# Kernel optimization log

Measured on AMD Instinct MI355X. Metric: run time of the kernel, lower is better.

The kernel has to match this reference:

```python
import jax, jax.numpy as jnp
import numpy as np

NEG_INF = -9e15  # matches torch reference mask value
LEAKY_SLOPE = 0.2  # alpha passed to nn.LeakyReLU


def setup_inputs() -> dict:
    key = jax.random.key(0)
    k1, k2, k3 = jax.random.split(key, 3)
    B, N, E = 256, 300, 100
    item_embeddings = jax.random.normal(k1, (B, N, E), dtype=jnp.float32)
    adj = jax.random.randint(k2, (B, N, N), 0, 5, dtype=jnp.int64)  # edge types 0..4
    A = jax.random.normal(k3, (4, E), dtype=jnp.float32)  # stacked a_0..a_3
    return {"item_embeddings": item_embeddings, "adj": adj, "A": A}


def reference(item_embeddings, adj, A):
    h = item_embeddings  # [B, N, E]
    # Original: a_input[b,i,j,:] = h[b,i,:] * h[b,j,:]; e_k = leakyrelu(a_input @ a_k).
    # Equivalent without the (B,N,N,E) tensor: e_k[b,i,j] = lrelu(sum_d h[b,i,d] h[b,j,d] A[k,d]).
    e = jnp.einsum('bid,bjd,kd->kbij', h, h, A)  # [4, B, N, N]
    e = jax.nn.leaky_relu(e, LEAKY_SLOPE)
    mask = jnp.full_like(e[0], NEG_INF)
    alpha = jnp.where(adj == 1, e[0], mask)
    alpha = jnp.where(adj == 2, e[1], alpha)
    alpha = jnp.where(adj == 3, e[2], alpha)
    alpha = jnp.where(adj == 4, e[3], alpha)
    alpha = jax.nn.softmax(alpha, axis=-1)
    return jnp.matmul(alpha, h)  # [B, N, E]
```

## Files before the change

kernel.cpp:

```cpp
#include <hip/hip_runtime.h>


typedef _Float16 half8 __attribute__((ext_vector_type(8)));
typedef _Float16 half4 __attribute__((ext_vector_type(4)));
typedef float f32x4 __attribute__((ext_vector_type(4)));

constexpr int B_ = 256, N_ = 300, E_ = 100;
constexpr float NEGINF = -9e15f;
constexpr float PADV   = -3e38f;

constexpr int LDS_BYTES = 68096 + 1024;

__global__ __launch_bounds__(640)
void gat_flash6(const float* __restrict__ H, const int* __restrict__ ADJ,
                const float* __restrict__ A, float* __restrict__ OUT) {
  extern __shared__ char smraw[];
  _Float16* hS  = (_Float16*)smraw;
  _Float16* A16 = (_Float16*)(smraw + 68096);

  const int bid = blockIdx.x;
  const int b = bid >> 1, q = bid & 1;
  const int tid = threadIdx.x;
  const int w = tid >> 6, lane = tid & 63;
  const int lg = lane >> 4, ll = lane & 15;

  const float* Hb  = H + (size_t)b * (N_ * E_);
  const int*   AJb = ADJ + (size_t)b * (N_ * N_);

  for (int u = tid; u < 304 * 14; u += 640) {
    const int j = u / 14, hr = u % 14;
    half8 v;
#pragma unroll
    for (int e = 0; e < 8; ++e) {
      const int d = hr * 8 + e;
      v[e] = (_Float16)((j < N_ && d < E_) ? Hb[j * E_ + d] : 0.f);
    }
    *(half8*)&hS[(((j >> 4) * 7 + (hr >> 1)) << 8) + ((j & 15) << 4) + ((hr & 1) << 3)] = v;
  }
  if (tid < 64) {
    const int k = tid >> 4, oct = tid & 15;
    half8 v;
#pragma unroll
    for (int e = 0; e < 8; ++e) {
      const int d = oct * 8 + e;
      v[e] = (_Float16)((d < E_) ? A[k * E_ + d] : 0.f);
    }
    *(half8*)&A16[k * 128 + oct * 8] = v;
  }
  __syncthreads();

  const unsigned ldsbase = (unsigned)(size_t)(void*)hS;
  const unsigned trlane  = (unsigned)(ll * 8 + lg * 128);

  const int s = 2 * w + q;
  if (s < 19) {
    const int irow = s * 16 + ll;
    const int irc  = irow < N_ ? irow : N_ - 1;

    half8 g[3][4];
    half4 gt[4];
#pragma unroll
    for (int db = 0; db < 3; ++db) {
      const int doct = db * 4 + lg;
      const half8 hi = *(const half8*)&hS[((s * 7 + (doct >> 1)) << 8) + (ll << 4) + ((doct & 1) << 3)];
#pragma unroll
      for (int k = 0; k < 4; ++k)
        g[db][k] = hi * *(const half8*)&A16[k * 128 + doct * 8];
    }
    {
      const half4 hit = *(const half4*)&hS[((s * 7 + 6) << 8) + (ll << 4) + lg * 4];
#pragma unroll
      for (int k = 0; k < 4; ++k)
        gt[k] = hit * *(const half4*)&A16[k * 128 + 96 + lg * 4];
    }

    float m = PADV, lsum = 0.f;
    f32x4 acc[7];
#pragma unroll
    for (int t = 0; t < 7; ++t) acc[t] = (f32x4){0.f, 0.f, 0.f, 0.f};

    const int* ajrow = AJb + (size_t)irc * N_;
    int4 av = *(const int4*)(ajrow + lg * 4);

    for (int jt = 0; jt < 19; ++jt) {
      int4 avn = av;
      if (jt < 18) {
        int jc = jt * 16 + 16 + lg * 4;
        if (jc > N_ - 4) jc = N_ - 4;
        avn = *(const int4*)(ajrow + jc);
      }

      f32x4 c0 = {0.f, 0.f, 0.f, 0.f}, c1 = c0, c2 = c0, c3 = c0;
#pragma unroll
      for (int db = 0; db < 3; ++db) {
        const int doct = db * 4 + lg;
        const half8 aj = *(const half8*)&hS[((jt * 7 + (doct >> 1)) << 8) + (ll << 4) + ((doct & 1) << 3)];
        c0 = __builtin_amdgcn_mfma_f32_16x16x32_f16(aj, g[db][0], c0, 0, 0, 0);
        c1 = __builtin_amdgcn_mfma_f32_16x16x32_f16(aj, g[db][1], c1, 0, 0, 0);
        c2 = __builtin_amdgcn_mfma_f32_16x16x32_f16(aj, g[db][2], c2, 0, 0, 0);
        c3 = __builtin_amdgcn_mfma_f32_16x16x32_f16(aj, g[db][3], c3, 0, 0, 0);
      }
      {
        const half4 ajt = *(const half4*)&hS[((jt * 7 + 6) << 8) + (ll << 4) + lg * 4];
        c0 = __builtin_amdgcn_mfma_f32_16x16x16f16(ajt, gt[0], c0, 0, 0, 0);
        c1 = __builtin_amdgcn_mfma_f32_16x16x16f16(ajt, gt[1], c1, 0, 0, 0);
        c2 = __builtin_amdgcn_mfma_f32_16x16x16f16(ajt, gt[2], c2, 0, 0, 0);
        c3 = __builtin_amdgcn_mfma_f32_16x16x16f16(ajt, gt[3], c3, 0, 0, 0);
      }

      const unsigned trb = ldsbase + (unsigned)(jt * 3584) + trlane;
      half4 hf[7];
#pragma unroll
      for (int t = 0; t < 7; ++t)
        asm volatile("ds_read_b64_tr_b16 %0, %1 offset:%2"
                     : "=v"(hf[t]) : "v"(trb), "i"(t * 512));

      const int va[4] = {av.x, av.y, av.z, av.w};
      float sv[4];
#pragma unroll
      for (int r = 0; r < 4; ++r) {
        const float e = (va[r] == 1) ? c0[r] : (va[r] == 2) ? c1[r]
                       : (va[r] == 3) ? c2[r] : c3[r];
        sv[r] = (va[r] == 0) ? NEGINF : fmaxf(e, 0.2f * e);
      }
      if (jt == 18 && lg == 3) { sv[0] = PADV; sv[1] = PADV; sv[2] = PADV; sv[3] = PADV; }
      av = avn;

      float tmax = fmaxf(fmaxf(sv[0], sv[1]), fmaxf(sv[2], sv[3]));
      tmax = fmaxf(tmax, __shfl_xor(tmax, 16));
      tmax = fmaxf(tmax, __shfl_xor(tmax, 32));
      if (tmax > m) {
        const float f = __expf(m - tmax);
        m = tmax;
        lsum *= f;
#pragma unroll
        for (int t = 0; t < 7; ++t) {
          acc[t][0] *= f; acc[t][1] *= f; acc[t][2] *= f; acc[t][3] *= f;
        }
      }
      const float p0 = __expf(sv[0] - m), p1 = __expf(sv[1] - m);
      const float p2 = __expf(sv[2] - m), p3 = __expf(sv[3] - m);
      lsum += (p0 + p1) + (p2 + p3);
      half4 pb;
      pb[0] = (_Float16)p0; pb[1] = (_Float16)p1;
      pb[2] = (_Float16)p2; pb[3] = (_Float16)p3;

      asm volatile("s_waitcnt lgkmcnt(0)" ::: "memory");
      __builtin_amdgcn_sched_barrier(0);
#pragma unroll
      for (int t = 0; t < 7; ++t)
        acc[t] = __builtin_amdgcn_mfma_f32_16x16x16f16(hf[t], pb, acc[t], 0, 0, 0);
    }

    lsum += __shfl_xor(lsum, 16);
    lsum += __shfl_xor(lsum, 32);
    const float rv = 1.f / lsum;
    if (irow < N_) {
      float* orow = OUT + ((size_t)b * N_ + irow) * E_;
#pragma unroll
      for (int t = 0; t < 7; ++t) {
        const int e0 = t * 16 + lg * 4;
        if (e0 < E_) {
          f32x4 o = acc[t];
          o[0] *= rv; o[1] *= rv; o[2] *= rv; o[3] *= rv;
          *(f32x4*)&orow[e0] = o;
        }
      }
    }
  }
}

extern "C" void kernel_launch(void* const* d_in, const int* in_sizes, int n_in,
                              void* d_out, int out_size, void* d_ws, size_t ws_size,
                              hipStream_t stream) {
  const float* H  = (const float*)d_in[0];
  const int*   AJ = (const int*)d_in[1];
  const float* A  = (const float*)d_in[2];
  float* OUT = (float*)d_out;

  (void)hipFuncSetAttribute(reinterpret_cast<const void*>(gat_flash6),
                            hipFuncAttributeMaxDynamicSharedMemorySize,
                            LDS_BYTES);
  gat_flash6<<<2 * B_, 640, LDS_BYTES, stream>>>(H, AJ, A, OUT);
}
```

Baseline: 84.08 us.

## Merge batch blocks, double-buffer score operands, and use lazy exp2 softmax rescale

```diff
diff --git a/kernel.cpp b/kernel.cpp
--- a/kernel.cpp
+++ b/kernel.cpp
@@ -8,18 +8,91 @@
 constexpr int B_ = 256, N_ = 300, E_ = 100;
 constexpr float NEGINF = -9e15f;
 constexpr float PADV   = -3e38f;
+constexpr float LOG2E  = 1.44269504088896f;
 
 constexpr int LDS_BYTES = 68096 + 1024;
 
-__global__ __launch_bounds__(640)
-void gat_flash6(const float* __restrict__ H, const int* __restrict__ ADJ,
-                const float* __restrict__ A, float* __restrict__ OUT) {
+#define DSB128(dst, addr, off) \
+  asm volatile("ds_read_b128 %0, %1 offset:" #off : "=v"(dst) : "v"(addr))
+#define DSB64(dst, addr, off) \
+  asm volatile("ds_read_b64 %0, %1 offset:" #off : "=v"(dst) : "v"(addr))
+#define TRD(dst, addr, off) \
+  asm volatile("ds_read_b64_tr_b16 %0, %1 offset:" #off : "=v"(dst) : "v"(addr))
+#define LGKM0 do { asm volatile("s_waitcnt lgkmcnt(0)" ::: "memory"); \
+                   __builtin_amdgcn_sched_barrier(0); } while (0)
+
+#define SCORE16(AJ0, AJ1, AJ2, AJT)                                            \
+  c0 = __builtin_amdgcn_mfma_f32_16x16x32_f16(AJ0, g[0][0], c0, 0, 0, 0);      \
+  c1 = __builtin_amdgcn_mfma_f32_16x16x32_f16(AJ0, g[0][1], c1, 0, 0, 0);      \
+  c2 = __builtin_amdgcn_mfma_f32_16x16x32_f16(AJ0, g[0][2], c2, 0, 0, 0);      \
+  c3 = __builtin_amdgcn_mfma_f32_16x16x32_f16(AJ0, g[0][3], c3, 0, 0, 0);      \
+  c0 = __builtin_amdgcn_mfma_f32_16x16x32_f16(AJ1, g[1][0], c0, 0, 0, 0);      \
+  c1 = __builtin_amdgcn_mfma_f32_16x16x32_f16(AJ1, g[1][1], c1, 0, 0, 0);      \
+  c2 = __builtin_amdgcn_mfma_f32_16x16x32_f16(AJ1, g[1][2], c2, 0, 0, 0);      \
+  c3 = __builtin_amdgcn_mfma_f32_16x16x32_f16(AJ1, g[1][3], c3, 0, 0, 0);      \
+  c0 = __builtin_amdgcn_mfma_f32_16x16x32_f16(AJ2, g[2][0], c0, 0, 0, 0);      \
+  c1 = __builtin_amdgcn_mfma_f32_16x16x32_f16(AJ2, g[2][1], c1, 0, 0, 0);      \
+  c2 = __builtin_amdgcn_mfma_f32_16x16x32_f16(AJ2, g[2][2], c2, 0, 0, 0);      \
+  c3 = __builtin_amdgcn_mfma_f32_16x16x32_f16(AJ2, g[2][3], c3, 0, 0, 0);      \
+  c0 = __builtin_amdgcn_mfma_f32_16x16x16f16(AJT, gt[0], c0, 0, 0, 0);         \
+  c1 = __builtin_amdgcn_mfma_f32_16x16x16f16(AJT, gt[1], c1, 0, 0, 0);         \
+  c2 = __builtin_amdgcn_mfma_f32_16x16x16f16(AJT, gt[2], c2, 0, 0, 0);         \
+  c3 = __builtin_amdgcn_mfma_f32_16x16x16f16(AJT, gt[3], c3, 0, 0, 0)
+
+#define TILE_SECTION(AJ0, AJ1, AJ2, AJT, NX0, NX1, NX2, NXT,                   \
+                     SO0, SO1, SO2, SOT, TO0, TO1, TO2, TO3, TO4, TO5, TO6,    \
+                     NJC)                                                      \
+  {                                                                            \
+    DSB128(NX0, aA, SO0); DSB128(NX1, aA, SO1); DSB128(NX2, aA, SO2);          \
+    DSB64(NXT, aT, SOT);                                                       \
+    int jcn_ = (NJC); if (jcn_ > N_ - 4) jcn_ = N_ - 4;                        \
+    const int4 avn_ = *(const int4*)(ajrow + jcn_);                            \
+    f32x4 c0 = {0.f, 0.f, 0.f, 0.f}, c1 = c0, c2 = c0, c3 = c0;                \
+    SCORE16(AJ0, AJ1, AJ2, AJT);                                               \
+    TRD(tr[0], aR, TO0); TRD(tr[1], aR, TO1); TRD(tr[2], aR, TO2);             \
+    TRD(tr[3], aR, TO3); TRD(tr[4], aR, TO4); TRD(tr[5], aR, TO5);             \
+    TRD(tr[6], aR, TO6);                                                       \
+    const int va[4] = {av.x, av.y, av.z, av.w};                                \
+    float sv[4];                                                               \
+    _Pragma("unroll")                                                          \
+    for (int r = 0; r < 4; ++r) {                                              \
+      const float e = (va[r] == 1) ? c0[r] : (va[r] == 2) ? c1[r]              \
+                     : (va[r] == 3) ? c2[r] : c3[r];                           \
+      sv[r] = (va[r] == 0) ? NEGINF : fmaxf(e, 0.2f * e);                      \
+    }                                                                          \
+    const float lmax = fmaxf(fmaxf(sv[0], sv[1]), fmaxf(sv[2], sv[3]));        \
+    if (__any(lmax > m + 8.f)) {                                               \
+      float tmax = fmaxf(lmax, __shfl_xor(lmax, 16));                          \
+      tmax = fmaxf(tmax, __shfl_xor(tmax, 32));                                \
+      const float nm = fmaxf(m, tmax);                                         \
+      const float f = exp2f(m - nm);                                           \
+      m = nm; lsum *= f;                                                       \
+      _Pragma("unroll")                                                        \
+      for (int t = 0; t < 7; ++t) {                                            \
+        acc[t][0] *= f; acc[t][1] *= f; acc[t][2] *= f; acc[t][3] *= f;        \
+      }                                                                        \
+    }                                                                          \
+    const float p0_ = exp2f(sv[0] - m), p1_ = exp2f(sv[1] - m);                \
+    const float p2_ = exp2f(sv[2] - m), p3_ = exp2f(sv[3] - m);                \
+    lsum += (p0_ + p1_) + (p2_ + p3_);                                         \
+    half4 pb;                                                                  \
+    pb[0] = (_Float16)p0_; pb[1] = (_Float16)p1_;                              \
+    pb[2] = (_Float16)p2_; pb[3] = (_Float16)p3_;                              \
+    LGKM0;                                                                     \
+    _Pragma("unroll")                                                          \
+    for (int t = 0; t < 7; ++t)                                                \
+      acc[t] = __builtin_amdgcn_mfma_f32_16x16x16f16(tr[t], pb, acc[t], 0, 0, 0); \
+    av = avn_;                                                                 \
+  }
+
+__global__ __launch_bounds__(768)
+void gat_flash13(const float* __restrict__ H, const int* __restrict__ ADJ,
+                 const float* __restrict__ A, float* __restrict__ OUT) {
   extern __shared__ char smraw[];
   _Float16* hS  = (_Float16*)smraw;
   _Float16* A16 = (_Float16*)(smraw + 68096);
 
-  const int bid = blockIdx.x;
-  const int b = bid >> 1, q = bid & 1;
+  const int b = blockIdx.x;
   const int tid = threadIdx.x;
   const int w = tid >> 6, lane = tid & 63;
   const int lg = lane >> 4, ll = lane & 15;
@@ -27,7 +100,7 @@
   const float* Hb  = H + (size_t)b * (N_ * E_);
   const int*   AJb = ADJ + (size_t)b * (N_ * N_);
 
-  for (int u = tid; u < 304 * 14; u += 640) {
+  for (int u = tid; u < 304 * 14; u += 768) {
     const int j = u / 14, hr = u % 14;
     half8 v;
 #pragma unroll
@@ -43,17 +116,15 @@
 #pragma unroll
     for (int e = 0; e < 8; ++e) {
       const int d = oct * 8 + e;
-      v[e] = (_Float16)((d < E_) ? A[k * E_ + d] : 0.f);
+      v[e] = (_Float16)((d < E_) ? A[k * E_ + d] * LOG2E : 0.f);
     }
     *(half8*)&A16[k * 128 + oct * 8] = v;
   }
   __syncthreads();
 
   const unsigned ldsbase = (unsigned)(size_t)(void*)hS;
-  const unsigned trlane  = (unsigned)(ll * 8 + lg * 128);
-
-  const int s = 2 * w + q;
-  if (s < 19) {
+
+  for (int s = w; s < 19; s += 12) {
     const int irow = s * 16 + ll;
     const int irc  = irow < N_ ? irow : N_ - 1;
 
@@ -82,39 +153,36 @@
     const int* ajrow = AJb + (size_t)irc * N_;
     int4 av = *(const int4*)(ajrow + lg * 4);
 
-    for (int jt = 0; jt < 19; ++jt) {
-      int4 avn = av;
-      if (jt < 18) {
-        int jc = jt * 16 + 16 + lg * 4;
-        if (jc > N_ - 4) jc = N_ - 4;
-        avn = *(const int4*)(ajrow + jc);
-      }
-
+    unsigned aA = ldsbase + ((unsigned)(lg >> 1) << 9) + ((unsigned)ll << 5) + ((unsigned)(lg & 1) << 4);
+    unsigned aT = ldsbase + ((unsigned)ll << 5) + ((unsigned)lg << 3);
+    unsigned aR = ldsbase + ((unsigned)ll << 3) + ((unsigned)lg << 7);
+
+    half8 A0, A1, A2; half4 At;
+    half8 B0, B1, B2; half4 Bt;
+    half4 tr[7];
+
+    DSB128(A0, aA, 0); DSB128(A1, aA, 1024); DSB128(A2, aA, 2048);
+    DSB64(At, aT, 3072);
+    LGKM0;
+
+    for (int p = 0; p < 9; ++p) {
+      TILE_SECTION(A0, A1, A2, At, B0, B1, B2, Bt,
+                   3584, 4608, 5632, 6656,
+                   0, 512, 1024, 1536, 2048, 2560, 3072,
+                   p * 32 + 16 + lg * 4);
+      TILE_SECTION(B0, B1, B2, Bt, A0, A1, A2, At,
+                   7168, 8192, 9216, 10240,
+                   3584, 4096, 4608, 5120, 5632, 6144, 6656,
+                   p * 32 + 32 + lg * 4);
+      aA += 7168; aT += 7168; aR += 7168;
+    }
+
+    {
       f32x4 c0 = {0.f, 0.f, 0.f, 0.f}, c1 = c0, c2 = c0, c3 = c0;
-#pragma unroll
-      for (int db = 0; db < 3; ++db) {
-        const int doct = db * 4 + lg;
-        const half8 aj = *(const half8*)&hS[((jt * 7 + (doct >> 1)) << 8) + (ll << 4) + ((doct & 1) << 3)];
-        c0 = __builtin_amdgcn_mfma_f32_16x16x32_f16(aj, g[db][0], c0, 0, 0, 0);
-        c1 = __builtin_amdgcn_mfma_f32_16x16x32_f16(aj, g[db][1], c1, 0, 0, 0);
-        c2 = __builtin_amdgcn_mfma_f32_16x16x32_f16(aj, g[db][2], c2, 0, 0, 0);
-        c3 = __builtin_amdgcn_mfma_f32_16x16x32_f16(aj, g[db][3], c3, 0, 0, 0);
-      }
-      {
-        const half4 ajt = *(const half4*)&hS[((jt * 7 + 6) << 8) + (ll << 4) + lg * 4];
-        c0 = __builtin_amdgcn_mfma_f32_16x16x16f16(ajt, gt[0], c0, 0, 0, 0);
-        c1 = __builtin_amdgcn_mfma_f32_16x16x16f16(ajt, gt[1], c1, 0, 0, 0);
-        c2 = __builtin_amdgcn_mfma_f32_16x16x16f16(ajt, gt[2], c2, 0, 0, 0);
-        c3 = __builtin_amdgcn_mfma_f32_16x16x16f16(ajt, gt[3], c3, 0, 0, 0);
-      }
-
-      const unsigned trb = ldsbase + (unsigned)(jt * 3584) + trlane;
-      half4 hf[7];
-#pragma unroll
-      for (int t = 0; t < 7; ++t)
-        asm volatile("ds_read_b64_tr_b16 %0, %1 offset:%2"
-                     : "=v"(hf[t]) : "v"(trb), "i"(t * 512));
-
+      SCORE16(A0, A1, A2, At);
+      TRD(tr[0], aR, 0);    TRD(tr[1], aR, 512);  TRD(tr[2], aR, 1024);
+      TRD(tr[3], aR, 1536); TRD(tr[4], aR, 2048); TRD(tr[5], aR, 2560);
+      TRD(tr[6], aR, 3072);
       const int va[4] = {av.x, av.y, av.z, av.w};
       float sv[4];
 #pragma unroll
@@ -123,33 +191,29 @@
                        : (va[r] == 3) ? c2[r] : c3[r];
         sv[r] = (va[r] == 0) ? NEGINF : fmaxf(e, 0.2f * e);
       }
-      if (jt == 18 && lg == 3) { sv[0] = PADV; sv[1] = PADV; sv[2] = PADV; sv[3] = PADV; }
-      av = avn;
-
-      float tmax = fmaxf(fmaxf(sv[0], sv[1]), fmaxf(sv[2], sv[3]));
-      tmax = fmaxf(tmax, __shfl_xor(tmax, 16));
-      tmax = fmaxf(tmax, __shfl_xor(tmax, 32));
-      if (tmax > m) {
-        const float f = __expf(m - tmax);
-        m = tmax;
-        lsum *= f;
+      if (lg == 3) { sv[0] = PADV; sv[1] = PADV; sv[2] = PADV; sv[3] = PADV; }
+      const float lmax = fmaxf(fmaxf(sv[0], sv[1]), fmaxf(sv[2], sv[3]));
+      if (__any(lmax > m + 8.f)) {
+        float tmax = fmaxf(lmax, __shfl_xor(lmax, 16));
+        tmax = fmaxf(tmax, __shfl_xor(tmax, 32));
+        const float nm = fmaxf(m, tmax);
+        const float f = exp2f(m - nm);
+        m = nm; lsum *= f;
 #pragma unroll
         for (int t = 0; t < 7; ++t) {
           acc[t][0] *= f; acc[t][1] *= f; acc[t][2] *= f; acc[t][3] *= f;
         }
       }
-      const float p0 = __expf(sv[0] - m), p1 = __expf(sv[1] - m);
-      const float p2 = __expf(sv[2] - m), p3 = __expf(sv[3] - m);
+      const float p0 = exp2f(sv[0] - m), p1 = exp2f(sv[1] - m);
+      const float p2 = exp2f(sv[2] - m), p3 = exp2f(sv[3] - m);
       lsum += (p0 + p1) + (p2 + p3);
       half4 pb;
       pb[0] = (_Float16)p0; pb[1] = (_Float16)p1;
       pb[2] = (_Float16)p2; pb[3] = (_Float16)p3;
-
-      asm volatile("s_waitcnt lgkmcnt(0)" ::: "memory");
-      __builtin_amdgcn_sched_barrier(0);
+      LGKM0;
 #pragma unroll
       for (int t = 0; t < 7; ++t)
-        acc[t] = __builtin_amdgcn_mfma_f32_16x16x16f16(hf[t], pb, acc[t], 0, 0, 0);
+        acc[t] = __builtin_amdgcn_mfma_f32_16x16x16f16(tr[t], pb, acc[t], 0, 0, 0);
     }
 
     lsum += __shfl_xor(lsum, 16);
@@ -178,8 +242,8 @@
   const float* A  = (const float*)d_in[2];
   float* OUT = (float*)d_out;
 
-  (void)hipFuncSetAttribute(reinterpret_cast<const void*>(gat_flash6),
+  (void)hipFuncSetAttribute(reinterpret_cast<const void*>(gat_flash13),
                             hipFuncAttributeMaxDynamicSharedMemorySize,
                             LDS_BYTES);
-  gat_flash6<<<2 * B_, 640, LDS_BYTES, stream>>>(H, AJ, A, OUT);
+  gat_flash13<<<B_, 768, LDS_BYTES, stream>>>(H, AJ, A, OUT);
 }
```

Measured after the change: 69.88 us. 1.2x faster.

## Use one 1024-thread block per batch with split-K for leftover row strips

Applied to the files above, without the earlier changes.

```diff
diff --git a/kernel.cpp b/kernel.cpp
--- a/kernel.cpp
+++ b/kernel.cpp
@@ -8,18 +8,25 @@
 constexpr int B_ = 256, N_ = 300, E_ = 100;
 constexpr float NEGINF = -9e15f;
 constexpr float PADV   = -3e38f;
-
-constexpr int LDS_BYTES = 68096 + 1024;
-
-__global__ __launch_bounds__(640)
-void gat_flash6(const float* __restrict__ H, const int* __restrict__ ADJ,
-                const float* __restrict__ A, float* __restrict__ OUT) {
+constexpr float LOG2E  = 1.44269504088896f;
+
+constexpr int PART_OFF  = 69120;
+constexpr int LDS_BYTES = 69120 + 9 * 7680;
+
+#define TRD(dst, addr, off) \
+  asm volatile("ds_read_b64_tr_b16 %0, %1 offset:" #off : "=v"(dst) : "v"(addr))
+#define LGKM0 do { asm volatile("s_waitcnt lgkmcnt(0)" ::: "memory"); \
+                   __builtin_amdgcn_sched_barrier(0); } while (0)
+
+__global__ __launch_bounds__(1024)
+void gat_flash14(const float* __restrict__ H, const int* __restrict__ ADJ,
+                 const float* __restrict__ A, float* __restrict__ OUT) {
   extern __shared__ char smraw[];
-  _Float16* hS  = (_Float16*)smraw;
-  _Float16* A16 = (_Float16*)(smraw + 68096);
-
-  const int bid = blockIdx.x;
-  const int b = bid >> 1, q = bid & 1;
+  _Float16* hS   = (_Float16*)smraw;
+  _Float16* A16  = (_Float16*)(smraw + 68096);
+  float*    part = (float*)(smraw + PART_OFF);
+
+  const int b = blockIdx.x;
   const int tid = threadIdx.x;
   const int w = tid >> 6, lane = tid & 63;
   const int lg = lane >> 4, ll = lane & 15;
@@ -27,7 +34,7 @@
   const float* Hb  = H + (size_t)b * (N_ * E_);
   const int*   AJb = ADJ + (size_t)b * (N_ * N_);
 
-  for (int u = tid; u < 304 * 14; u += 640) {
+  for (int u = tid; u < 304 * 14; u += 1024) {
     const int j = u / 14, hr = u % 14;
     half8 v;
 #pragma unroll
@@ -43,7 +50,7 @@
 #pragma unroll
     for (int e = 0; e < 8; ++e) {
       const int d = oct * 8 + e;
-      v[e] = (_Float16)((d < E_) ? A[k * E_ + d] : 0.f);
+      v[e] = (_Float16)((d < E_) ? A[k * E_ + d] * LOG2E : 0.f);
     }
     *(half8*)&A16[k * 128 + oct * 8] = v;
   }
@@ -52,13 +59,16 @@
   const unsigned ldsbase = (unsigned)(size_t)(void*)hS;
   const unsigned trlane  = (unsigned)(ll * 8 + lg * 128);
 
-  const int s = 2 * w + q;
-  if (s < 19) {
+  half8 g[3][4];
+  half4 gt[4];
+  float m, lsum;
+  f32x4 acc[7];
+  const int* ajrow = AJb;
+
+  auto prep_strip = [&](int s) {
     const int irow = s * 16 + ll;
     const int irc  = irow < N_ ? irow : N_ - 1;
-
-    half8 g[3][4];
-    half4 gt[4];
+    ajrow = AJb + (size_t)irc * N_;
 #pragma unroll
     for (int db = 0; db < 3; ++db) {
       const int doct = db * 4 + lg;
@@ -67,94 +77,85 @@
       for (int k = 0; k < 4; ++k)
         g[db][k] = hi * *(const half8*)&A16[k * 128 + doct * 8];
     }
+    const half4 hit = *(const half4*)&hS[((s * 7 + 6) << 8) + (ll << 4) + lg * 4];
+#pragma unroll
+    for (int k = 0; k < 4; ++k)
+      gt[k] = hit * *(const half4*)&A16[k * 128 + 96 + lg * 4];
+    m = PADV; lsum = 0.f;
+#pragma unroll
+    for (int t = 0; t < 7; ++t) acc[t] = (f32x4){0.f, 0.f, 0.f, 0.f};
+  };
+
+  auto load_adj = [&](int jt) -> int4 {
+    int jc = jt * 16 + lg * 4;
+    if (jc > N_ - 4) jc = N_ - 4;
+    return *(const int4*)(ajrow + jc);
+  };
+
+  auto tile_body = [&](int jt, int4 av, bool tail) {
+    f32x4 c0 = {0.f, 0.f, 0.f, 0.f}, c1 = c0, c2 = c0, c3 = c0;
+#pragma unroll
+    for (int db = 0; db < 3; ++db) {
+      const int doct = db * 4 + lg;
+      const half8 aj = *(const half8*)&hS[((jt * 7 + (doct >> 1)) << 8) + (ll << 4) + ((doct & 1) << 3)];
+      c0 = __builtin_amdgcn_mfma_f32_16x16x32_f16(aj, g[db][0], c0, 0, 0, 0);
+      c1 = __builtin_amdgcn_mfma_f32_16x16x32_f16(aj, g[db][1], c1, 0, 0, 0);
+      c2 = __builtin_amdgcn_mfma_f32_16x16x32_f16(aj, g[db][2], c2, 0, 0, 0);
+      c3 = __builtin_amdgcn_mfma_f32_16x16x32_f16(aj, g[db][3], c3, 0, 0, 0);
+    }
     {
-      const half4 hit = *(const half4*)&hS[((s * 7 + 6) << 8) + (ll << 4) + lg * 4];
-#pragma unroll
-      for (int k = 0; k < 4; ++k)
-        gt[k] = hit * *(const half4*)&A16[k * 128 + 96 + lg * 4];
-    }
-
-    float m = PADV, lsum = 0.f;
-    f32x4 acc[7];
-#pragma unroll
-    for (int t = 0; t < 7; ++t) acc[t] = (f32x4){0.f, 0.f, 0.f, 0.f};
-
-    const int* ajrow = AJb + (size_t)irc * N_;
-    int4 av = *(const int4*)(ajrow + lg * 4);
-
-    for (int jt = 0; jt < 19; ++jt) {
-      int4 avn = av;
-      if (jt < 18) {
-        int jc = jt * 16 + 16 + lg * 4;
-        if (jc > N_ - 4) jc = N_ - 4;
-        avn = *(const int4*)(ajrow + jc);
-      }
-
-      f32x4 c0 = {0.f, 0.f, 0.f, 0.f}, c1 = c0, c2 = c0, c3 = c0;
-#pragma unroll
-      for (int db = 0; db < 3; ++db) {
-        const int doct = db * 4 + lg;
-        const half8 aj = *(const half8*)&hS[((jt * 7 + (doct >> 1)) << 8) + (ll << 4) + ((doct & 1) << 3)];
-        c0 = __builtin_amdgcn_mfma_f32_16x16x32_f16(aj, g[db][0], c0, 0, 0, 0);
-        c1 = __builtin_amdgcn_mfma_f32_16x16x32_f16(aj, g[db][1], c1, 0, 0, 0);
-        c2 = __builtin_amdgcn_mfma_f32_16x16x32_f16(aj, g[db][2], c2, 0, 0, 0);
-        c3 = __builtin_amdgcn_mfma_f32_16x16x32_f16(aj, g[db][3], c3, 0, 0, 0);
-      }
-      {
-        const half4 ajt = *(const half4*)&hS[((jt * 7 + 6) << 8) + (ll << 4) + lg * 4];
-        c0 = __builtin_amdgcn_mfma_f32_16x16x16f16(ajt, gt[0], c0, 0, 0, 0);
-        c1 = __builtin_amdgcn_mfma_f32_16x16x16f16(ajt, gt[1], c1, 0, 0, 0);
-        c2 = __builtin_amdgcn_mfma_f32_16x16x16f16(ajt, gt[2], c2, 0, 0, 0);
-        c3 = __builtin_amdgcn_mfma_f32_16x16x16f16(ajt, gt[3], c3, 0, 0, 0);
-      }
-
-      const unsigned trb = ldsbase + (unsigned)(jt * 3584) + trlane;
-      half4 hf[7];
-#pragma unroll
-      for (int t = 0; t < 7; ++t)
-        asm volatile("ds_read_b64_tr_b16 %0, %1 offset:%2"
-                     : "=v"(hf[t]) : "v"(trb), "i"(t * 512));
-
-      const int va[4] = {av.x, av.y, av.z, av.w};
-      float sv[4];
-#pragma unroll
-      for (int r = 0; r < 4; ++r) {
-        const float e = (va[r] == 1) ? c0[r] : (va[r] == 2) ? c1[r]
-                       : (va[r] == 3) ? c2[r] : c3[r];
-        sv[r] = (va[r] == 0) ? NEGINF : fmaxf(e, 0.2f * e);
-      }
-      if (jt == 18 && lg == 3) { sv[0] = PADV; sv[1] = PADV; sv[2] = PADV; sv[3] = PADV; }
-      av = avn;
-
-      float tmax = fmaxf(fmaxf(sv[0], sv[1]), fmaxf(sv[2], sv[3]));
-      tmax = fmaxf(tmax, __shfl_xor(tmax, 16));
+      const half4 ajt = *(const half4*)&hS[((jt * 7 + 6) << 8) + (ll << 4) + lg * 4];
+      c0 = __builtin_amdgcn_mfma_f32_16x16x16f16(ajt, gt[0], c0, 0, 0, 0);
+      c1 = __builtin_amdgcn_mfma_f32_16x16x16f16(ajt, gt[1], c1, 0, 0, 0);
+      c2 = __builtin_amdgcn_mfma_f32_16x16x16f16(ajt, gt[2], c2, 0, 0, 0);
+      c3 = __builtin_amdgcn_mfma_f32_16x16x16f16(ajt, gt[3], c3, 0, 0, 0);
+    }
+    const int va[4] = {av.x, av.y, av.z, av.w};
+    float sv[4];
+#pragma unroll
+    for (int r = 0; r < 4; ++r) {
+      const float e = (va[r] == 1) ? c0[r] : (va[r] == 2) ? c1[r]
+                     : (va[r] == 3) ? c2[r] : c3[r];
+      sv[r] = (va[r] == 0) ? NEGINF : fmaxf(e, 0.2f * e);
+    }
+    if (tail && lg == 3) { sv[0] = PADV; sv[1] = PADV; sv[2] = PADV; sv[3] = PADV; }
+
+    const unsigned trb = ldsbase + (unsigned)(jt * 3584) + trlane;
+    half4 tr[7];
+    TRD(tr[0], trb, 0);    TRD(tr[1], trb, 512);  TRD(tr[2], trb, 1024);
+    TRD(tr[3], trb, 1536); TRD(tr[4], trb, 2048); TRD(tr[5], trb, 2560);
+    TRD(tr[6], trb, 3072);
+
+    const float lmax = fmaxf(fmaxf(sv[0], sv[1]), fmaxf(sv[2], sv[3]));
+    if (__any(lmax > m + 8.f)) {
+      float tmax = fmaxf(lmax, __shfl_xor(lmax, 16));
       tmax = fmaxf(tmax, __shfl_xor(tmax, 32));
-      if (tmax > m) {
-        const float f = __expf(m - tmax);
-        m = tmax;
-        lsum *= f;
-#pragma unroll
-        for (int t = 0; t < 7; ++t) {
-          acc[t][0] *= f; acc[t][1] *= f; acc[t][2] *= f; acc[t][3] *= f;
-        }
-      }
-      const float p0 = __expf(sv[0] - m), p1 = __expf(sv[1] - m);
-      const float p2 = __expf(sv[2] - m), p3 = __expf(sv[3] - m);
-      lsum += (p0 + p1) + (p2 + p3);
-      half4 pb;
-      pb[0] = (_Float16)p0; pb[1] = (_Float16)p1;
-      pb[2] = (_Float16)p2; pb[3] = (_Float16)p3;
-
-      asm volatile("s_waitcnt lgkmcnt(0)" ::: "memory");
-      __builtin_amdgcn_sched_barrier(0);
-#pragma unroll
-      for (int t = 0; t < 7; ++t)
-        acc[t] = __builtin_amdgcn_mfma_f32_16x16x16f16(hf[t], pb, acc[t], 0, 0, 0);
-    }
-
+      const float nm = fmaxf(m, tmax);
+      const float f = exp2f(m - nm);
+      m = nm; lsum *= f;
+#pragma unroll
+      for (int t = 0; t < 7; ++t) {
+        acc[t][0] *= f; acc[t][1] *= f; acc[t][2] *= f; acc[t][3] *= f;
+      }
+    }
+    const float p0 = exp2f(sv[0] - m), p1 = exp2f(sv[1] - m);
+    const float p2 = exp2f(sv[2] - m), p3 = exp2f(sv[3] - m);
+    lsum += (p0 + p1) + (p2 + p3);
+    half4 pb;
+    pb[0] = (_Float16)p0; pb[1] = (_Float16)p1;
+    pb[2] = (_Float16)p2; pb[3] = (_Float16)p3;
+
+    LGKM0;
+#pragma unroll
+    for (int t = 0; t < 7; ++t)
+      acc[t] = __builtin_amdgcn_mfma_f32_16x16x16f16(tr[t], pb, acc[t], 0, 0, 0);
+  };
+
+  auto store_rows = [&](int s) {
     lsum += __shfl_xor(lsum, 16);
     lsum += __shfl_xor(lsum, 32);
     const float rv = 1.f / lsum;
+    const int irow = s * 16 + ll;
     if (irow < N_) {
       float* orow = OUT + ((size_t)b * N_ + irow) * E_;
 #pragma unroll
@@ -167,6 +168,65 @@
         }
       }
     }
+  };
+
+  prep_strip(w);
+  {
+    int4 av = load_adj(0);
+    for (int jt = 0; jt < 18; ++jt) {
+      const int4 nv = load_adj(jt + 1);
+      tile_body(jt, av, false);
+      av = nv;
+    }
+    tile_body(18, av, true);
+  }
+  store_rows(w);
+
+  if (w < 12) {
+    const int t = w >> 2, q = w & 3;
+    const int s2 = 16 + t;
+    prep_strip(s2);
+    const int j0 = q * 5;
+    const int j1 = (q < 3) ? (j0 + 5) : 18;
+    int4 av = load_adj(j0);
+    for (int jt = j0; jt < j1; ++jt) {
+      const int4 nv = load_adj(jt + 1);
+      tile_body(jt, av, false);
+      av = nv;
+    }
+    if (q == 3) tile_body(18, av, true);
+
+    if (q) {
+      float* dst = part + (size_t)(t * 3 + (q - 1)) * 1920 + lane * 30;
+#pragma unroll
+      for (int tt = 0; tt < 7; ++tt) {
+        dst[4 * tt + 0] = acc[tt][0]; dst[4 * tt + 1] = acc[tt][1];
+        dst[4 * tt + 2] = acc[tt][2]; dst[4 * tt + 3] = acc[tt][3];
+      }
+      dst[28] = m; dst[29] = lsum;
+    }
+  }
+  __syncthreads();
+
+  if (w < 12 && (w & 3) == 0) {
+    const int t = w >> 2;
+#pragma unroll
+    for (int q = 1; q <= 3; ++q) {
+      const float* src = part + (size_t)(t * 3 + (q - 1)) * 1920 + lane * 30;
+      const float mq = src[28], lq = src[29];
+      const float M  = fmaxf(m, mq);
+      const float f0 = exp2f(m - M), f1 = exp2f(mq - M);
+      m = M;
+      lsum = lsum * f0 + lq * f1;
+#pragma unroll
+      for (int tt = 0; tt < 7; ++tt) {
+        acc[tt][0] = acc[tt][0] * f0 + src[4 * tt + 0] * f1;
+        acc[tt][1] = acc[tt][1] * f0 + src[4 * tt + 1] * f1;
+        acc[tt][2] = acc[tt][2] * f0 + src[4 * tt + 2] * f1;
+        acc[tt][3] = acc[tt][3] * f0 + src[4 * tt + 3] * f1;
+      }
+    }
+    store_rows(16 + t);
   }
 }
 
@@ -178,8 +238,8 @@
   const float* A  = (const float*)d_in[2];
   float* OUT = (float*)d_out;
 
-  (void)hipFuncSetAttribute(reinterpret_cast<const void*>(gat_flash6),
+  (void)hipFuncSetAttribute(reinterpret_cast<const void*>(gat_flash14),
                             hipFuncAttributeMaxDynamicSharedMemorySize,
                             LDS_BYTES);
-  gat_flash6<<<2 * B_, 640, LDS_BYTES, stream>>>(H, AJ, A, OUT);
+  gat_flash14<<<B_, 1024, LDS_BYTES, stream>>>(H, AJ, A, OUT);
 }
```

Result: no change. 83.28 us (-1.0%).
